# Kernel tuning notes

Measured on AMD Instinct MI355X. Metric: run time of the kernel, lower is better.

Reference implementation:

```python
import jax, jax.numpy as jnp
import numpy as np

N_NODES = 500_000
N_EDGES = 16_000_000
D_COEF = 1  # init arg d
EPS = 1e-12  # F.normalize eps


def setup_inputs() -> dict:
    key = jax.random.key(0)
    k1, k2, k3 = jax.random.split(key, 3)
    theta = jax.random.normal(k1, (N_NODES, 1), dtype=jnp.float32)
    src = jax.random.randint(k2, (N_EDGES,), 0, N_NODES, dtype=jnp.int64)
    dst = jax.random.randint(k3, (N_EDGES,), 0, N_NODES, dtype=jnp.int64)
    v0 = jnp.ones((), dtype=jnp.float32)
    w0 = jnp.ones((), dtype=jnp.float32)
    return {"theta": theta, "src": src, "dst": dst, "v0": v0, "w0": w0}


def reference(theta, src, dst, v0, w0):
    # node velocity: v0 * [cos(theta), sin(theta)]  -> [N, 2]
    v = v0 * jnp.concatenate((jnp.cos(theta), jnp.sin(theta)), axis=-1)

    # edge message: dtheta = (theta_src - theta_dst) * d ; m = [cos, sin] -> [E, 2]
    dtheta = (theta[src, 0] - theta[dst, 0]) * D_COEF  # [E]
    m = jnp.stack((jnp.cos(dtheta), jnp.sin(dtheta)), axis=-1)  # [E, 2]

    # mailbox mean over incoming edges per destination node (segment mean)
    msum = jax.ops.segment_sum(m, dst, num_segments=N_NODES)  # [N, 2]
    cnt = jax.ops.segment_sum(jnp.ones((dst.shape[0],), m.dtype), dst,
                              num_segments=N_NODES)  # [N]
    mean_cs = msum / jnp.maximum(cnt, 1.0)[:, None]  # [N, 2]

    # torque: w0 * normalize(mean_cs, dim=-1)[..., 1:2]
    norm = jnp.linalg.norm(mean_cs, axis=-1, keepdims=True)
    unit = mean_cs / jnp.maximum(norm, EPS)
    torque = w0 * unit[:, 1:2]  # [N, 1]
    return v, torque
```

## Files before the change

kernel.cpp:

```cpp
#include <hip/hip_runtime.h>
#include <hip/hip_bf16.h>
#include <math.h>


#define NBITS_Q   21
#define Q_MASK    ((1u << NBITS_Q) - 1)
#define Q_SCALE   131072.0f
#define Q_INV     (1.0f / 131072.0f)
#define BIN_SHIFT 11
#define BIN_W     2048
#define NB        245
#define CAP       67584
#define K_BATCH   4096
#define EPT       16
#define CSTR      16
#define SCALE_F   524288.0f
#define INV_SCALE (1.0f / 524288.0f)
#define INV_2PI   0.15915494309189535f

typedef unsigned uint4_v __attribute__((ext_vector_type(4)));

__global__ void init_cursors(unsigned* __restrict__ cur, int cstride) {
    const int tid = threadIdx.x;
    for (int i = tid; i < 256 * CSTR; i += 256) cur[i] = 0u;
    __syncthreads();
    if (tid < NB) cur[tid * cstride] = (unsigned)tid * CAP;
}

__global__ __launch_bounds__(256) void bin_edges_sort(
        const float* __restrict__ theta,
        const int4* __restrict__ src4, const int4* __restrict__ dst4,
        unsigned* __restrict__ bins, unsigned* __restrict__ cursor,
        int E, int cstride)
{
    __shared__ unsigned      sorted[K_BATCH];
    __shared__ unsigned char sbin[K_BATCH];
    __shared__ unsigned      hist[256];
    __shared__ unsigned      base[256];
    __shared__ unsigned      gbase[256];
    __shared__ unsigned      lcnt[256];

    const int tid   = threadIdx.x;
    const int bb    = blockIdx.x;
    const int e0    = bb * K_BATCH;
    const int nval  = min(K_BATCH, E - e0);
    const int E4    = E >> 2;
    const int base4 = e0 >> 2;

    hist[tid] = 0u;
    lcnt[tid] = 0u;
    __syncthreads();

    int4 sQ[EPT / 4];
#pragma unroll
    for (int j = 0; j < EPT / 4; ++j) {
        const int idx4 = base4 + j * 256 + tid;
        sQ[j] = (idx4 < E4) ? src4[idx4] : make_int4(0, 0, 0, 0);
    }
    float tq[EPT];
#pragma unroll
    for (int j = 0; j < EPT / 4; ++j) {
        tq[j * 4 + 0] = theta[sQ[j].x];
        tq[j * 4 + 1] = theta[sQ[j].y];
        tq[j * 4 + 2] = theta[sQ[j].z];
        tq[j * 4 + 3] = theta[sQ[j].w];
    }

    unsigned ent[EPT];
    unsigned bn[EPT];
#pragma unroll
    for (int j = 0; j < EPT / 4; ++j) {
        const int idx4 = base4 + j * 256 + tid;
        const int q0   = j * 4;
        if (idx4 < E4) {
            const int4 d = dst4[idx4];
            const int dd[4] = {d.x, d.y, d.z, d.w};
#pragma unroll
            for (int k = 0; k < 4; ++k) {
                const unsigned b = (unsigned)dd[k] >> BIN_SHIFT;
                float qf = (tq[q0 + k] + 8.0f) * Q_SCALE + 0.5f;
                qf = fminf(fmaxf(qf, 0.0f), 2097151.0f);
                ent[q0 + k] = ((unsigned)(dd[k] & (BIN_W - 1)) << NBITS_Q)
                              | (unsigned)qf;
                bn[q0 + k]  = b;
                atomicAdd(&hist[b], 1u);
            }
        } else {
#pragma unroll
            for (int k = 0; k < 4; ++k) bn[q0 + k] = 0xFFu;
        }
    }
    __syncthreads();

    if (tid < 64) {
        unsigned h[4];
#pragma unroll
        for (int k = 0; k < 4; ++k) h[k] = hist[tid * 4 + k];
        const unsigned tot = h[0] + h[1] + h[2] + h[3];
        unsigned s = tot;
#pragma unroll
        for (int off = 1; off < 64; off <<= 1) {
            const unsigned y = __shfl_up(s, off);
            if (tid >= off) s += y;
        }
        unsigned run = s - tot;
#pragma unroll
        for (int k = 0; k < 4; ++k) {
            base[tid * 4 + k] = run;
            run += h[k];
        }
#pragma unroll
        for (int k = 0; k < 4; ++k)
            if (h[k]) gbase[tid * 4 + k] =
                atomicAdd(&cursor[(tid * 4 + k) * cstride], h[k]);
    }
    __syncthreads();

#pragma unroll
    for (int q = 0; q < EPT; ++q) {
        if (bn[q] != 0xFFu) {
            const unsigned b   = bn[q];
            const unsigned pos = base[b] + atomicAdd(&lcnt[b], 1u);
            sorted[pos] = ent[q];
            sbin[pos]   = (unsigned char)b;
        }
    }
    __syncthreads();

    for (int l = tid; l < nval; l += 256) {
        const unsigned b    = sbin[l];
        const unsigned gpos = gbase[b] + ((unsigned)l - base[b]);
        if (gpos < (b + 1u) * CAP)
            bins[gpos] = sorted[l];
    }
}

__global__ __launch_bounds__(1024) void reduce_bins(
        const float* __restrict__ theta, const unsigned* __restrict__ bins,
        const unsigned* __restrict__ cursor, const float* __restrict__ v0p,
        const float* __restrict__ w0p, float* __restrict__ out,
        int N, int cstride)
{
    __shared__ float th[BIN_W];
    __shared__ unsigned long long acc[BIN_W];
    const int b     = blockIdx.x;
    const int tid   = threadIdx.x;
    const int node0 = b * BIN_W;
    const int W     = min(BIN_W, N - node0);

    for (int j = tid; j < BIN_W; j += 1024) {
        th[j]  = (j < W) ? theta[node0 + j] : 0.f;
        acc[j] = 0ull;
    }
    __syncthreads();

    const unsigned  base  = (unsigned)b * CAP;
    const int       count = (int)(cursor[b * cstride] - base);
    const unsigned* bp    = bins + base;

    const int CH = 1024 * 8;
    int i0 = 0;
    for (; i0 + CH <= count; i0 += CH) {
        const uint4_v ea = __builtin_nontemporal_load(
            (const uint4_v*)(bp + i0 + tid * 4));
        const uint4_v eb = __builtin_nontemporal_load(
            (const uint4_v*)(bp + i0 + 4096 + tid * 4));
        const unsigned ee[8] = {ea.x, ea.y, ea.z, ea.w, eb.x, eb.y, eb.z, eb.w};
#pragma unroll
        for (int k = 0; k < 8; ++k) {
            const unsigned e = ee[k];
            const unsigned l = e >> NBITS_Q;
            const float ts = (float)(e & Q_MASK) * Q_INV - 8.0f;
            const float r  = (ts - th[l]) * INV_2PI;
            const float sn = __builtin_amdgcn_sinf(r);
            const float cs = __builtin_amdgcn_cosf(r);
            const unsigned cq = (unsigned)((cs + 1.0f) * SCALE_F + 0.5f);
            const unsigned sq = (unsigned)((sn + 1.0f) * SCALE_F + 0.5f);
            atomicAdd(&acc[l], (1ull << 56) | ((unsigned long long)cq << 28)
                               | (unsigned long long)sq);
        }
    }
    for (int i = i0 + tid; i < count; i += 1024) {
        const unsigned e = __builtin_nontemporal_load(bp + i);
        const unsigned l = e >> NBITS_Q;
        const float ts = (float)(e & Q_MASK) * Q_INV - 8.0f;
        const float r  = (ts - th[l]) * INV_2PI;
        const float sn = __builtin_amdgcn_sinf(r);
        const float cs = __builtin_amdgcn_cosf(r);
        const unsigned cq = (unsigned)((cs + 1.0f) * SCALE_F + 0.5f);
        const unsigned sq = (unsigned)((sn + 1.0f) * SCALE_F + 0.5f);
        atomicAdd(&acc[l], (1ull << 56) | ((unsigned long long)cq << 28)
                           | (unsigned long long)sq);
    }
    __syncthreads();

    const float v0 = *v0p, w0 = *w0p;
    for (int j = tid; j < W; j += 1024) {
        const float t  = th[j];
        const float rr = t * INV_2PI;
        const float sn = __builtin_amdgcn_sinf(rr);
        const float cs = __builtin_amdgcn_cosf(rr);
        ((float2*)out)[node0 + j] = make_float2(v0 * cs, v0 * sn);
        const unsigned long long P = acc[j];
        const float c  = (float)(unsigned)(P >> 56);
        const float xs = (float)(unsigned)((P >> 28) & 0xFFFFFFFull) * INV_SCALE - c;
        const float ys = (float)(unsigned)(P & 0xFFFFFFFull) * INV_SCALE - c;
        const float nrm = sqrtf(xs * xs + ys * ys);
        out[2 * N + node0 + j] = w0 * (ys / fmaxf(nrm, 1e-12f));
    }
}


__global__ void zero_ws_kernel(float4* __restrict__ ws, int n4) {
    int i = blockIdx.x * blockDim.x + threadIdx.x;
    if (i < n4) ws[i] = make_float4(0.f, 0.f, 0.f, 0.f);
}

__global__ void edge_kernel_fb(const float* __restrict__ theta,
                               const int4* __restrict__ src4,
                               const int4* __restrict__ dst4,
                               float2* __restrict__ acc, int E8) {
    int i = blockIdx.x * blockDim.x + threadIdx.x;
    if (i >= E8) return;
    const int4 s0 = src4[2 * i], s1 = src4[2 * i + 1];
    const int4 d0 = dst4[2 * i], d1 = dst4[2 * i + 1];
    const int ss[8] = {s0.x, s0.y, s0.z, s0.w, s1.x, s1.y, s1.z, s1.w};
    const int dd[8] = {d0.x, d0.y, d0.z, d0.w, d1.x, d1.y, d1.z, d1.w};
    float ts[8], td[8];
#pragma unroll
    for (int k = 0; k < 8; ++k) ts[k] = theta[ss[k]];
#pragma unroll
    for (int k = 0; k < 8; ++k) td[k] = theta[dd[k]];
#pragma unroll
    for (int k = 0; k < 8; ++k) {
        float sn, cs;
        __sincosf(ts[k] - td[k], &sn, &cs);
        atomicAdd(&acc[dd[k]].x, cs);
        atomicAdd(&acc[dd[k]].y, sn);
    }
}

__global__ void node_kernel_fb(const float* __restrict__ theta,
                               const float2* __restrict__ acc,
                               const float* __restrict__ v0p,
                               const float* __restrict__ w0p,
                               float* __restrict__ out, int N) {
    int i = blockIdx.x * blockDim.x + threadIdx.x;
    if (i >= N) return;
    const float v0 = *v0p, w0 = *w0p;
    float sn, cs;
    __sincosf(theta[i], &sn, &cs);
    ((float2*)out)[i] = make_float2(v0 * cs, v0 * sn);
    const float2 a = acc[i];
    const float nrm = sqrtf(a.x * a.x + a.y * a.y);
    out[2 * N + i] = w0 * (a.y / fmaxf(nrm, 1e-12f));
}

extern "C" void kernel_launch(void* const* d_in, const int* in_sizes, int n_in,
                              void* d_out, int out_size, void* d_ws, size_t ws_size,
                              hipStream_t stream) {
    const float* theta = (const float*)d_in[0];
    const int*   src   = (const int*)d_in[1];
    const int*   dst   = (const int*)d_in[2];
    const float* v0p   = (const float*)d_in[3];
    const float* w0p   = (const float*)d_in[4];
    float*       out   = (float*)d_out;

    const int N = in_sizes[0];
    const int E = in_sizes[1];

    const size_t bins_bytes = (size_t)NB * CAP * sizeof(unsigned);
    const size_t need_pad   = (size_t)256 * CSTR * 4 + bins_bytes;
    const size_t need_min   = 1024 + bins_bytes;

    const int nblk  = (E + K_BATCH - 1) / K_BATCH;
    const int nbins = (N + BIN_W - 1) / BIN_W;

    if (ws_size >= need_pad && N <= NB * BIN_W) {
        unsigned* cursor = (unsigned*)d_ws;
        unsigned* bins   = cursor + 256 * CSTR;

        init_cursors<<<1, 256, 0, stream>>>(cursor, CSTR);
        bin_edges_sort<<<nblk, 256, 0, stream>>>(theta, (const int4*)src,
                                                 (const int4*)dst,
                                                 bins, cursor, E, CSTR);
        reduce_bins<<<nbins, 1024, 0, stream>>>(theta, bins, cursor,
                                                v0p, w0p, out, N, CSTR);
    } else if (ws_size >= need_min && N <= NB * BIN_W) {
        unsigned* cursor = (unsigned*)d_ws;
        unsigned* bins   = cursor + 256;

        init_cursors<<<1, 256, 0, stream>>>(cursor, 1);
        bin_edges_sort<<<nblk, 256, 0, stream>>>(theta, (const int4*)src,
                                                 (const int4*)dst,
                                                 bins, cursor, E, 1);
        reduce_bins<<<nbins, 1024, 0, stream>>>(theta, bins, cursor,
                                                v0p, w0p, out, N, 1);
    } else {
        float2* acc = (float2*)d_ws;
        {
            const int n4 = (2 * N) / 4;
            zero_ws_kernel<<<(n4 + 255) / 256, 256, 0, stream>>>((float4*)d_ws, n4);
        }
        {
            const int E8 = E / 8;
            edge_kernel_fb<<<(E8 + 255) / 256, 256, 0, stream>>>(
                theta, (const int4*)src, (const int4*)dst, acc, E8);
        }
        node_kernel_fb<<<(N + 255) / 256, 256, 0, stream>>>(theta, acc, v0p, w0p,
                                                            out, N);
    }
}
```

Before: 284.8 us.

## Fuse binning and per-bin reduction into one persistent producer/consumer kernel

Replaces the separate sort and reduce launches with one kernel. Reducer blocks (one per node bin) wait on per-group completion counters that 512 producer blocks raise as they bin 8192-edge chunks, so reduction of early groups overlaps with binning of later ones. Bins are split into 4 group segments with per-group cursors, and nontemporal loads are dropped. The scheme depends on all reducer and producer blocks being co-resident, since reducers spin on global flags; if they are not, the kernel can deadlock. The old bin_edges_sort path is also edited so its per-thread arrays now hold 32 entries while K_BATCH is 8192.

New measurement: 730.8 us. +156.6%, slower.

```diff
diff --git a/kernel.cpp b/kernel.cpp
--- a/kernel.cpp
+++ b/kernel.cpp
@@ -10,21 +10,243 @@
 #define BIN_SHIFT 11
 #define BIN_W     2048
 #define NB        245
-#define CAP       67584
-#define K_BATCH   4096
+#define K_BATCH   8192
 #define EPT       16
-#define CSTR      16
+#define NTHREADS  512
+#define NPROD     512
+#define GROUPS    4
+#define GSHIFT    9
+#define SEG_CAP   17888
 #define SCALE_F   524288.0f
 #define INV_SCALE (1.0f / 524288.0f)
 #define INV_2PI   0.15915494309189535f
+#define CAP       67584
+#define CSTR      16
 
 typedef unsigned uint4_v __attribute__((ext_vector_type(4)));
 
-__global__ void init_cursors(unsigned* __restrict__ cur, int cstride) {
+__global__ void init_fused(unsigned* __restrict__ ws_u32) {
+    const int i = blockIdx.x * blockDim.x + threadIdx.x;
+    if (i < 2048) ws_u32[i] = 0u;
+}
+
+__global__ __launch_bounds__(512, 6) void fused_sort_reduce(
+        const float* __restrict__ theta,
+        const int4* __restrict__ src4, const int4* __restrict__ dst4,
+        unsigned* __restrict__ bins, unsigned* __restrict__ cur,
+        unsigned* __restrict__ done, const float* __restrict__ v0p,
+        const float* __restrict__ w0p, float* __restrict__ out,
+        int N, int E)
+{
+    __shared__ __align__(16) unsigned char pool[45056];
+    const int tid    = threadIdx.x;
+    const int NCHUNK = (E + K_BATCH - 1) / K_BATCH;
+
+    if (blockIdx.x < NB) {
+        float*              th  = (float*)pool;
+        unsigned long long* acc = (unsigned long long*)(pool + 8192);
+        const int b     = blockIdx.x;
+        const int node0 = b * BIN_W;
+        const int W     = min(BIN_W, N - node0);
+
+        for (int j = tid; j < BIN_W; j += NTHREADS) {
+            th[j]  = (j < W) ? theta[node0 + j] : 0.f;
+            acc[j] = 0ull;
+        }
+        __syncthreads();
+
+        for (int g = 0; g < GROUPS; ++g) {
+            const unsigned target =
+                (unsigned)min(1 << GSHIFT, NCHUNK - (g << GSHIFT));
+            if (tid == 0) {
+                while (__hip_atomic_load(&done[g * 16], __ATOMIC_ACQUIRE,
+                                         __HIP_MEMORY_SCOPE_AGENT) < target)
+                    __builtin_amdgcn_s_sleep(8);
+            }
+            __syncthreads();
+            const unsigned craw = __hip_atomic_load(
+                &cur[b * GROUPS + g], __ATOMIC_ACQUIRE,
+                __HIP_MEMORY_SCOPE_AGENT);
+            const int cnt = (int)(craw < (unsigned)SEG_CAP ? craw
+                                                           : (unsigned)SEG_CAP);
+            const unsigned* bp =
+                bins + (size_t)(b * GROUPS + g) * SEG_CAP;
+
+            const int CH = NTHREADS * 8;
+            int i0 = 0;
+            for (; i0 + CH <= cnt; i0 += CH) {
+                const uint4_v ea = *(const uint4_v*)(bp + i0 + tid * 4);
+                const uint4_v eb = *(const uint4_v*)(bp + i0 + NTHREADS * 4
+                                                     + tid * 4);
+                const unsigned ee[8] = {ea.x, ea.y, ea.z, ea.w,
+                                        eb.x, eb.y, eb.z, eb.w};
+#pragma unroll
+                for (int k = 0; k < 8; ++k) {
+                    const unsigned e = ee[k];
+                    const unsigned l = e >> NBITS_Q;
+                    const float ts = (float)(e & Q_MASK) * Q_INV - 8.0f;
+                    const float r  = (ts - th[l]) * INV_2PI;
+                    const float sn = __builtin_amdgcn_sinf(r);
+                    const float cs = __builtin_amdgcn_cosf(r);
+                    const unsigned cq =
+                        (unsigned)((cs + 1.0f) * SCALE_F + 0.5f);
+                    const unsigned sq =
+                        (unsigned)((sn + 1.0f) * SCALE_F + 0.5f);
+                    atomicAdd(&acc[l], (1ull << 56)
+                              | ((unsigned long long)cq << 28)
+                              | (unsigned long long)sq);
+                }
+            }
+            for (int i = i0 + tid; i < cnt; i += NTHREADS) {
+                const unsigned e = bp[i];
+                const unsigned l = e >> NBITS_Q;
+                const float ts = (float)(e & Q_MASK) * Q_INV - 8.0f;
+                const float r  = (ts - th[l]) * INV_2PI;
+                const float sn = __builtin_amdgcn_sinf(r);
+                const float cs = __builtin_amdgcn_cosf(r);
+                const unsigned cq = (unsigned)((cs + 1.0f) * SCALE_F + 0.5f);
+                const unsigned sq = (unsigned)((sn + 1.0f) * SCALE_F + 0.5f);
+                atomicAdd(&acc[l], (1ull << 56)
+                          | ((unsigned long long)cq << 28)
+                          | (unsigned long long)sq);
+            }
+        }
+        __syncthreads();
+
+        const float v0 = *v0p, w0 = *w0p;
+        for (int j = tid; j < W; j += NTHREADS) {
+            const float t  = th[j];
+            const float rr = t * INV_2PI;
+            const float sn = __builtin_amdgcn_sinf(rr);
+            const float cs = __builtin_amdgcn_cosf(rr);
+            ((float2*)out)[node0 + j] = make_float2(v0 * cs, v0 * sn);
+            const unsigned long long P = acc[j];
+            const float c  = (float)(unsigned)(P >> 56);
+            const float xs =
+                (float)(unsigned)((P >> 28) & 0xFFFFFFFull) * INV_SCALE - c;
+            const float ys =
+                (float)(unsigned)(P & 0xFFFFFFFull) * INV_SCALE - c;
+            const float nrm = sqrtf(xs * xs + ys * ys);
+            out[2 * N + node0 + j] = w0 * (ys / fmaxf(nrm, 1e-12f));
+        }
+    } else {
+        unsigned*      sorted = (unsigned*)pool;
+        unsigned char* sbin   = pool + 32768;
+        unsigned*      hist   = (unsigned*)(pool + 40960);
+        unsigned*      base_  = hist + 256;
+        unsigned*      gbase  = base_ + 256;
+        unsigned*      lcnt   = gbase + 256;
+
+        const int pid = blockIdx.x - NB;
+        const int E4  = E >> 2;
+
+        for (int c = pid; c < NCHUNK; c += NPROD) {
+            const int g = c >> GSHIFT;
+            if (tid < 256) { hist[tid] = 0u; lcnt[tid] = 0u; }
+            __syncthreads();
+
+            const int base4 = c * (K_BATCH >> 2);
+            int4 sQ[EPT / 4];
+#pragma unroll
+            for (int j = 0; j < EPT / 4; ++j) {
+                const int idx4 = base4 + j * NTHREADS + tid;
+                sQ[j] = (idx4 < E4) ? src4[idx4] : make_int4(0, 0, 0, 0);
+            }
+            float tq[EPT];
+#pragma unroll
+            for (int j = 0; j < EPT / 4; ++j) {
+                tq[j * 4 + 0] = theta[sQ[j].x];
+                tq[j * 4 + 1] = theta[sQ[j].y];
+                tq[j * 4 + 2] = theta[sQ[j].z];
+                tq[j * 4 + 3] = theta[sQ[j].w];
+            }
+
+            unsigned ent[EPT];
+            unsigned bn[EPT];
+#pragma unroll
+            for (int j = 0; j < EPT / 4; ++j) {
+                const int idx4 = base4 + j * NTHREADS + tid;
+                const int q0   = j * 4;
+                if (idx4 < E4) {
+                    const int4 d = dst4[idx4];
+                    const int dd[4] = {d.x, d.y, d.z, d.w};
+#pragma unroll
+                    for (int k = 0; k < 4; ++k) {
+                        const unsigned bb = (unsigned)dd[k] >> BIN_SHIFT;
+                        float qf = (tq[q0 + k] + 8.0f) * Q_SCALE + 0.5f;
+                        qf = fminf(fmaxf(qf, 0.0f), 2097151.0f);
+                        ent[q0 + k] =
+                            ((unsigned)(dd[k] & (BIN_W - 1)) << NBITS_Q)
+                            | (unsigned)qf;
+                        bn[q0 + k] = bb;
+                        atomicAdd(&hist[bb], 1u);
+                    }
+                } else {
+#pragma unroll
+                    for (int k = 0; k < 4; ++k) bn[q0 + k] = 0xFFu;
+                }
+            }
+            __syncthreads();
+
+            if (tid < 64) {
+                unsigned h[4];
+#pragma unroll
+                for (int k = 0; k < 4; ++k) h[k] = hist[tid * 4 + k];
+                const unsigned tot = h[0] + h[1] + h[2] + h[3];
+                unsigned s = tot;
+#pragma unroll
+                for (int off = 1; off < 64; off <<= 1) {
+                    const unsigned y = __shfl_up(s, off);
+                    if (tid >= off) s += y;
+                }
+                unsigned run = s - tot;
+#pragma unroll
+                for (int k = 0; k < 4; ++k) {
+                    base_[tid * 4 + k] = run;
+                    run += h[k];
+                }
+#pragma unroll
+                for (int k = 0; k < 4; ++k)
+                    if (h[k]) gbase[tid * 4 + k] =
+                        atomicAdd(&cur[(tid * 4 + k) * GROUPS + g], h[k]);
+            }
+            __syncthreads();
+
+#pragma unroll
+            for (int q = 0; q < EPT; ++q) {
+                if (bn[q] != 0xFFu) {
+                    const unsigned bb  = bn[q];
+                    const unsigned pos = base_[bb] + atomicAdd(&lcnt[bb], 1u);
+                    sorted[pos] = ent[q];
+                    sbin[pos]   = (unsigned char)bb;
+                }
+            }
+            __syncthreads();
+
+            const int nval = min(K_BATCH, E - c * K_BATCH);
+            for (int l = tid; l < nval; l += NTHREADS) {
+                const unsigned bb = sbin[l];
+                const unsigned gp = gbase[bb] + ((unsigned)l - base_[bb]);
+                if (gp < (unsigned)SEG_CAP)
+                    bins[(size_t)(bb * GROUPS + g) * SEG_CAP + gp] = sorted[l];
+            }
+            __syncthreads();
+
+            if (tid == 0) {
+                __threadfence();
+                __hip_atomic_fetch_add(&done[g * 16], 1u, __ATOMIC_RELEASE,
+                                       __HIP_MEMORY_SCOPE_AGENT);
+            }
+        }
+    }
+}
+
+
+__global__ void init_cursors(unsigned* __restrict__ curv, int cstride) {
     const int tid = threadIdx.x;
-    for (int i = tid; i < 256 * CSTR; i += 256) cur[i] = 0u;
-    __syncthreads();
-    if (tid < NB) cur[tid * cstride] = (unsigned)tid * CAP;
+    for (int i = tid; i < 256 * CSTR; i += 256) curv[i] = 0u;
+    __syncthreads();
+    if (tid < NB) curv[tid * cstride] = (unsigned)tid * CAP;
 }
 
 __global__ __launch_bounds__(256) void bin_edges_sort(
@@ -41,8 +263,7 @@
     __shared__ unsigned      lcnt[256];
 
     const int tid   = threadIdx.x;
-    const int bb    = blockIdx.x;
-    const int e0    = bb * K_BATCH;
+    const int e0    = blockIdx.x * K_BATCH;
     const int nval  = min(K_BATCH, E - e0);
     const int E4    = E >> 2;
     const int base4 = e0 >> 2;
@@ -51,25 +272,25 @@
     lcnt[tid] = 0u;
     __syncthreads();
 
-    int4 sQ[EPT / 4];
-#pragma unroll
-    for (int j = 0; j < EPT / 4; ++j) {
+    int4 sQ[8];
+#pragma unroll
+    for (int j = 0; j < 8; ++j) {
         const int idx4 = base4 + j * 256 + tid;
         sQ[j] = (idx4 < E4) ? src4[idx4] : make_int4(0, 0, 0, 0);
     }
-    float tq[EPT];
-#pragma unroll
-    for (int j = 0; j < EPT / 4; ++j) {
+    float tq[32];
+#pragma unroll
+    for (int j = 0; j < 8; ++j) {
         tq[j * 4 + 0] = theta[sQ[j].x];
         tq[j * 4 + 1] = theta[sQ[j].y];
         tq[j * 4 + 2] = theta[sQ[j].z];
         tq[j * 4 + 3] = theta[sQ[j].w];
     }
 
-    unsigned ent[EPT];
-    unsigned bn[EPT];
-#pragma unroll
-    for (int j = 0; j < EPT / 4; ++j) {
+    unsigned ent[32];
+    unsigned bn[32];
+#pragma unroll
+    for (int j = 0; j < 8; ++j) {
         const int idx4 = base4 + j * 256 + tid;
         const int q0   = j * 4;
         if (idx4 < E4) {
@@ -117,7 +338,7 @@
     __syncthreads();
 
 #pragma unroll
-    for (int q = 0; q < EPT; ++q) {
+    for (int q = 0; q < 32; ++q) {
         if (bn[q] != 0xFFu) {
             const unsigned b   = bn[q];
             const unsigned pos = base[b] + atomicAdd(&lcnt[b], 1u);
@@ -161,10 +382,8 @@
     const int CH = 1024 * 8;
     int i0 = 0;
     for (; i0 + CH <= count; i0 += CH) {
-        const uint4_v ea = __builtin_nontemporal_load(
-            (const uint4_v*)(bp + i0 + tid * 4));
-        const uint4_v eb = __builtin_nontemporal_load(
-            (const uint4_v*)(bp + i0 + 4096 + tid * 4));
+        const uint4_v ea = *(const uint4_v*)(bp + i0 + tid * 4);
+        const uint4_v eb = *(const uint4_v*)(bp + i0 + 4096 + tid * 4);
         const unsigned ee[8] = {ea.x, ea.y, ea.z, ea.w, eb.x, eb.y, eb.z, eb.w};
 #pragma unroll
         for (int k = 0; k < 8; ++k) {
@@ -181,7 +400,7 @@
         }
     }
     for (int i = i0 + tid; i < count; i += 1024) {
-        const unsigned e = __builtin_nontemporal_load(bp + i);
+        const unsigned e = bp[i];
         const unsigned l = e >> NBITS_Q;
         const float ts = (float)(e & Q_MASK) * Q_INV - 8.0f;
         const float r  = (ts - th[l]) * INV_2PI;
@@ -269,16 +488,25 @@
     const int N = in_sizes[0];
     const int E = in_sizes[1];
 
-    const size_t bins_bytes = (size_t)NB * CAP * sizeof(unsigned);
-    const size_t need_pad   = (size_t)256 * CSTR * 4 + bins_bytes;
-    const size_t need_min   = 1024 + bins_bytes;
-
-    const int nblk  = (E + K_BATCH - 1) / K_BATCH;
-    const int nbins = (N + BIN_W - 1) / BIN_W;
-
-    if (ws_size >= need_pad && N <= NB * BIN_W) {
+    const size_t need_fused = 8192 + (size_t)NB * GROUPS * SEG_CAP * 4;
+    const size_t need_r12   = (size_t)256 * CSTR * 4
+                              + (size_t)NB * CAP * 4;
+
+    if (ws_size >= need_fused && N <= NB * BIN_W
+        && E <= (GROUPS << GSHIFT) * K_BATCH) {
+        unsigned* cur  = (unsigned*)d_ws;
+        unsigned* done = cur + 1024;
+        unsigned* bins = cur + 2048;
+
+        init_fused<<<8, 256, 0, stream>>>(cur);
+        fused_sort_reduce<<<NB + NPROD, NTHREADS, 0, stream>>>(
+            theta, (const int4*)src, (const int4*)dst,
+            bins, cur, done, v0p, w0p, out, N, E);
+    } else if (ws_size >= need_r12 && N <= NB * BIN_W) {
         unsigned* cursor = (unsigned*)d_ws;
         unsigned* bins   = cursor + 256 * CSTR;
+        const int nblk   = (E + K_BATCH - 1) / K_BATCH;
+        const int nbins  = (N + BIN_W - 1) / BIN_W;
 
         init_cursors<<<1, 256, 0, stream>>>(cursor, CSTR);
         bin_edges_sort<<<nblk, 256, 0, stream>>>(theta, (const int4*)src,
@@ -286,16 +514,6 @@
                                                  bins, cursor, E, CSTR);
         reduce_bins<<<nbins, 1024, 0, stream>>>(theta, bins, cursor,
                                                 v0p, w0p, out, N, CSTR);
-    } else if (ws_size >= need_min && N <= NB * BIN_W) {
-        unsigned* cursor = (unsigned*)d_ws;
-        unsigned* bins   = cursor + 256;
-
-        init_cursors<<<1, 256, 0, stream>>>(cursor, 1);
-        bin_edges_sort<<<nblk, 256, 0, stream>>>(theta, (const int4*)src,
-                                                 (const int4*)dst,
-                                                 bins, cursor, E, 1);
-        reduce_bins<<<nbins, 1024, 0, stream>>>(theta, bins, cursor,
-                                                v0p, w0p, out, N, 1);
     } else {
         float2* acc = (float2*)d_ws;
         {
```
